# Optimization experiments

Measured on AMD Instinct MI355X. Metric: run time of the kernel, lower is better.

Reference implementation:

```python
import jax, jax.numpy as jnp
import numpy as np

NUM_LEVELS = 16
COARSEST = 16
FINEST = 1024
TABLE_SIZE = 524288  # max_hash_table_entries per level
FEAT = 2             # hash_table_feature_dim
DENSITY_W = 64
COLOR_W = 64
N_POINTS = 262144

PRIMES = jnp.array([1, 2654435761, 805459861], dtype=jnp.uint32)
# 8 cube corners: 1 -> ceil coordinate, 0 -> floor coordinate (matches source vertex_0..vertex_7)
CORNER_SEL = np.array([[1,1,1],[1,1,0],[1,0,1],[0,1,1],[1,0,0],[0,1,0],[0,0,1],[0,0,0]], dtype=bool)


def hash_encode(position, hash_table):
    # position: (N,3) in [0,1); hash_table: (NUM_LEVELS*TABLE_SIZE, FEAT)
    levels = jnp.arange(NUM_LEVELS)
    growth = jnp.exp((jnp.log(float(FINEST)) - jnp.log(float(COARSEST))) / (NUM_LEVELS - 1))
    scalings = jnp.floor(COARSEST * growth ** levels)            # (L,)
    scaled = position[:, None, :] * scalings[None, :, None]       # (N,L,3)
    floor = jnp.floor(scaled)
    ceil = jnp.ceil(scaled)
    sel = jnp.asarray(CORNER_SEL)[None, None]                     # (1,1,8,3)
    corners = jnp.where(sel, ceil[:, :, None, :], floor[:, :, None, :]).astype(jnp.uint32)  # (N,L,8,3)
    h = corners * PRIMES                                          # uint32 wrap-around mul
    idx = jnp.bitwise_xor(jnp.bitwise_xor(h[..., 0], h[..., 1]), h[..., 2]) % TABLE_SIZE
    idx = idx + (levels[None, :, None] * TABLE_SIZE).astype(jnp.uint32)  # (N,L,8)
    feats = hash_table[idx]                                       # (N,L,8,F) gather
    frac = scaled - floor                                         # (N,L,3)
    w = jnp.prod(jnp.where(sel, frac[:, :, None, :], 1.0 - frac[:, :, None, :]), axis=-1)  # (N,L,8)
    out = jnp.sum(feats * w[..., None], axis=2)                   # trilinear interp -> (N,L,F)
    return out.reshape(out.shape[0], NUM_LEVELS * FEAT)           # (N,32)


def sh_encode(d):
    # fourth-order spherical harmonics, vectorized over (N,3)
    x, y, z = d[:, 0], d[:, 1], d[:, 2]
    xx, yy, zz = x * x, y * y, z * z
    comps = [
        0.28209479177387814 * jnp.ones_like(x),
        0.4886025119029199 * y,
        0.4886025119029199 * z,
        0.4886025119029199 * x,
        1.0925484305920792 * x * y,
        1.0925484305920792 * y * z,
        0.9461746957575601 * zz - 0.31539156525252,
        1.0925484305920792 * x * z,
        0.5462742152960396 * (xx - yy),
        0.5900435899266435 * y * (3 * xx - yy),
        2.890611442640554 * x * y * z,
        0.4570457994644658 * y * (5 * zz - 1),
        0.3731763325901154 * z * (5 * zz - 3),
        0.4570457994644658 * x * (5 * zz - 1),
        1.445305721320277 * z * (xx - yy),
        0.5900435899266435 * x * (xx - 3 * yy),
    ]
    return jnp.stack(comps, axis=-1)  # (N,16)


def setup_inputs() -> dict:
    key = jax.random.key(0)
    ks = jax.random.split(key, 16)
    N = N_POINTS
    position = jax.random.uniform(ks[0], (N, 3), dtype=jnp.float32)
    direction = jax.random.normal(ks[1], (N, 3), dtype=jnp.float32)
    hash_table = jax.random.normal(ks[2], (NUM_LEVELS * TABLE_SIZE, FEAT), dtype=jnp.float32) * 1e-2
    enc_dim = NUM_LEVELS * FEAT  # 32
    def dense(k, fi, fo):
        return jax.random.normal(k, (fi, fo), dtype=jnp.float32) * (1.0 / np.sqrt(fi))
    return {
        "position": position,
        "direction": direction,
        "hash_table": hash_table,
        "w_d1": dense(ks[3], enc_dim, DENSITY_W), "b_d1": jnp.zeros((DENSITY_W,), jnp.float32),
        "w_d2": dense(ks[4], DENSITY_W, 16),      "b_d2": jnp.zeros((16,), jnp.float32),
        "w_c1": dense(ks[5], 16 + 16, COLOR_W),   "b_c1": jnp.zeros((COLOR_W,), jnp.float32),
        "w_c2": dense(ks[6], COLOR_W, COLOR_W),   "b_c2": jnp.zeros((COLOR_W,), jnp.float32),
        "w_c3": dense(ks[7], COLOR_W, 3),         "b_c3": jnp.zeros((3,), jnp.float32),
    }


def reference(position, direction, hash_table, w_d1, b_d1, w_d2, b_d2,
              w_c1, b_c1, w_c2, b_c2, w_c3, b_c3):
    enc_pos = hash_encode(position, hash_table)               # (N,32)
    h = jax.nn.relu(enc_pos @ w_d1 + b_d1)                    # (N,64)
    density = h @ w_d2 + b_d2                                 # (N,16)
    enc_dir = sh_encode(direction)                            # (N,16)
    x = jnp.concatenate([density, enc_dir], axis=-1)          # (N,32)
    x = jax.nn.relu(x @ w_c1 + b_c1)
    x = jax.nn.relu(x @ w_c2 + b_c2)
    x = x @ w_c3 + b_c3                                       # (N,3)
    color = jax.nn.sigmoid(x)                                 # high_dynamic_range=False
    return (density, color)
```

## Files before the change

### kernel.cpp

```cpp
#include <hip/hip_runtime.h>
#include <stdint.h>

#define NPTS 262144
#define TBL 524288u
#define TBL_MASK 524287u

#define WS_TAB_BYTES (16u * 524288u * 4u)
#define WS_ENC_OFF   WS_TAB_BYTES
#define WS_ENC_BYTES (16u * (uint32_t)NPTS * 4u)
#define WS_NEED      ((size_t)WS_TAB_BYTES + (size_t)WS_ENC_BYTES)

typedef __attribute__((ext_vector_type(8))) _Float16 half8;
typedef __attribute__((ext_vector_type(4))) float f32x4;

__device__ const float d_scale[16] = {16.f, 21.f, 27.f, 36.f, 48.f, 64.f, 84.f, 111.f,
                                      147.f, 194.f, 256.f, 337.f, 445.f, 588.f, 776.f, 1024.f};

__device__ __forceinline__ uint16_t f2h(float f) {
    _Float16 h = (_Float16)f;
    return __builtin_bit_cast(uint16_t, h);
}
__device__ __forceinline__ uint32_t pack2(float lo, float hi) {
    return (uint32_t)f2h(lo) | ((uint32_t)f2h(hi) << 16);
}
__device__ __forceinline__ float h2f_lo(uint32_t v) {
    return (float)__builtin_bit_cast(_Float16, (uint16_t)(v & 0xffffu));
}
__device__ __forceinline__ float h2f_hi(uint32_t v) {
    return (float)__builtin_bit_cast(_Float16, (uint16_t)(v >> 16));
}

__device__ __forceinline__ half8 bfrag(const float* __restrict__ W, int N, int kofs, int nofs, int l) {
    const int k0 = kofs + ((l >> 4) << 3);
    const float* p = W + (size_t)k0 * N + (nofs + (l & 15));
    union { uint32_t u[4]; half8 s; } r;
    r.u[0] = pack2(p[0 * N], p[1 * N]);
    r.u[1] = pack2(p[2 * N], p[3 * N]);
    r.u[2] = pack2(p[4 * N], p[5 * N]);
    r.u[3] = pack2(p[6 * N], p[7 * N]);
    return r.s;
}

__device__ __forceinline__ half8 bfrag3(const float* __restrict__ W, int kofs, int l) {
    const int k0 = kofs + ((l >> 4) << 3);
    const int n = l & 15;
    union { uint32_t u[4]; half8 s; } r;
    if (n < 3) {
        const float* p = W + (size_t)k0 * 3 + n;
        r.u[0] = pack2(p[0],  p[3]);
        r.u[1] = pack2(p[6],  p[9]);
        r.u[2] = pack2(p[12], p[15]);
        r.u[3] = pack2(p[18], p[21]);
    } else {
        r.u[0] = 0; r.u[1] = 0; r.u[2] = 0; r.u[3] = 0;
    }
    return r.s;
}

__device__ __forceinline__ half8 ld_a_h(const unsigned char* hcb, int mt, int kb, int l) {
    const int row = mt * 16 + (l & 15);
    uint32_t byte = (uint32_t)row * 128 + (uint32_t)kb * 64 + (uint32_t)((l >> 4) << 4);
    byte ^= (uint32_t)(row & 7) << 4;
    return *(const half8*)(hcb + byte);
}

__device__ __forceinline__ void st_h(unsigned char* hcb, int row, int col, float v) {
    uint32_t byte = (uint32_t)row * 128 + (uint32_t)col * 2;
    byte ^= (uint32_t)(row & 7) << 4;
    *(uint16_t*)(hcb + byte) = f2h(fmaxf(v, 0.f));
}

#define MFMA(a, b, c) __builtin_amdgcn_mfma_f32_16x16x32_f16((a), (b), (c), 0, 0, 0)

__global__ void __launch_bounds__(256) convert_tab(
    const float4* __restrict__ t, uint4* __restrict__ o, int n4)
{
    const int i = blockIdx.x * 256 + threadIdx.x;
    if (i < n4) {
        const float4 a = t[2 * i];
        const float4 b = t[2 * i + 1];
        o[i] = make_uint4(pack2(a.x, a.y), pack2(a.z, a.w),
                          pack2(b.x, b.y), pack2(b.z, b.w));
    }
}

__global__ void __launch_bounds__(256) gather_enc(
    const float* __restrict__ g_pos,
    const uint32_t* __restrict__ tab16,
    uint32_t* __restrict__ enc)
{
    const int b = blockIdx.x;
    const int x8 = b & 7;
    const int lev = (b >> 13) ? (15 - x8) : x8;
    const int p = (((b >> 3) & 1023) << 8) + threadIdx.x;

    const float px = g_pos[3 * p + 0];
    const float py = g_pos[3 * p + 1];
    const float pz = g_pos[3 * p + 2];

    const float s = d_scale[lev];
    const float sx = px * s, sy = py * s, sz = pz * s;
    const float fx = floorf(sx), fy = floorf(sy), fz = floorf(sz);
    const float cx = ceilf(sx),  cy = ceilf(sy),  cz = ceilf(sz);
    const float tx = sx - fx, ty = sy - fy, tz = sz - fz;
    const uint32_t x0 = (uint32_t)fx, x1 = (uint32_t)cx;
    const uint32_t hy0 = (uint32_t)fy * 2654435761u, hy1 = (uint32_t)cy * 2654435761u;
    const uint32_t hz0 = (uint32_t)fz * 805459861u,  hz1 = (uint32_t)cz * 805459861u;
    const bool xodd = (x0 & 1u) != 0u;

    const uint32_t* t = tab16 + (size_t)lev * TBL;
    float e0 = 0.f, e1 = 0.f;
    #pragma unroll
    for (int cp = 0; cp < 4; ++cp) {
        const uint32_t hyz = ((cp & 1) ? hy1 : hy0) ^ ((cp & 2) ? hz1 : hz0);
        const uint32_t idx0 = (x0 ^ hyz) & TBL_MASK;
        const uint32_t idx1 = (x1 ^ hyz) & TBL_MASK;
        const uint2 v2 = *reinterpret_cast<const uint2*>(t + (idx0 & ~1u));
        const bool lo = (idx0 & 1u) == 0u;
        const uint32_t v0 = lo ? v2.x : v2.y;
        uint32_t v1 = lo ? v2.y : v2.x;
        if (xodd) v1 = t[idx1];
        const float wyz = ((cp & 1) ? ty : 1.f - ty) * ((cp & 2) ? tz : 1.f - tz);
        const float w0 = (1.f - tx) * wyz;
        const float w1 = tx * wyz;
        e0 = fmaf(h2f_lo(v0), w0, fmaf(h2f_lo(v1), w1, e0));
        e1 = fmaf(h2f_hi(v0), w0, fmaf(h2f_hi(v1), w1, e1));
    }
    enc[(size_t)lev * NPTS + p] = pack2(e0, e1);
}

__global__ void __launch_bounds__(256, 3) nerf_mlp(
    const float* __restrict__ g_dir,
    const uint32_t* __restrict__ enc,
    const float* __restrict__ g_wd1,
    const float* __restrict__ g_bd1,
    const float* __restrict__ g_wd2,
    const float* __restrict__ g_bd2,
    const float* __restrict__ g_wc1,
    const float* __restrict__ g_bc1,
    const float* __restrict__ g_wc2,
    const float* __restrict__ g_bc2,
    const float* __restrict__ g_wc3,
    const float* __restrict__ g_bc3,
    float* __restrict__ g_out)
{
    __shared__ __align__(16) unsigned char s_lds[4 * 12288];
    unsigned char* wbase = s_lds + (threadIdx.x >> 6) * 12288;
    unsigned char* hcb  = wbase;
    unsigned char* xinb = wbase + 8192;

    const int l = threadIdx.x & 63;
    const int m_my = l >> 4;
    const int r_my = l & 15;
    const int wpt  = blockIdx.x * 256 + (threadIdx.x & 192);
    const int p    = wpt + l;

    #pragma unroll
    for (int kb = 0; kb < 4; ++kb) {
        uint4 w4;
        w4.x = enc[(size_t)(4 * kb + 0) * NPTS + p];
        w4.y = enc[(size_t)(4 * kb + 1) * NPTS + p];
        w4.z = enc[(size_t)(4 * kb + 2) * NPTS + p];
        w4.w = enc[(size_t)(4 * kb + 3) * NPTS + p];
        *(uint4*)(hcb + m_my * 1024 + (kb * 16 + r_my) * 16) = w4;
    }

    const float dx = g_dir[3 * p + 0];
    const float dy = g_dir[3 * p + 1];
    const float dz = g_dir[3 * p + 2];

    {
        const float xx = dx * dx, yy = dy * dy, zz = dz * dz;
        float s[16];
        s[0]  = 0.28209479177387814f;
        s[1]  = 0.4886025119029199f * dy;
        s[2]  = 0.4886025119029199f * dz;
        s[3]  = 0.4886025119029199f * dx;
        s[4]  = 1.0925484305920792f * dx * dy;
        s[5]  = 1.0925484305920792f * dy * dz;
        s[6]  = 0.9461746957575601f * zz - 0.31539156525252f;
        s[7]  = 1.0925484305920792f * dx * dz;
        s[8]  = 0.5462742152960396f * (xx - yy);
        s[9]  = 0.5900435899266435f * dy * (3.f * xx - yy);
        s[10] = 2.890611442640554f * dx * dy * dz;
        s[11] = 0.4570457994644658f * dy * (5.f * zz - 1.f);
        s[12] = 0.3731763325901154f * dz * (5.f * zz - 3.f);
        s[13] = 0.4570457994644658f * dx * (5.f * zz - 1.f);
        s[14] = 1.445305721320277f * dz * (xx - yy);
        s[15] = 0.5900435899266435f * dx * (xx - 3.f * yy);
        *(uint4*)(xinb + m_my * 1024 + (32 + r_my) * 16) =
            make_uint4(pack2(s[0], s[1]), pack2(s[2], s[3]), pack2(s[4], s[5]), pack2(s[6], s[7]));
        *(uint4*)(xinb + m_my * 1024 + (48 + r_my) * 16) =
            make_uint4(pack2(s[8], s[9]), pack2(s[10], s[11]), pack2(s[12], s[13]), pack2(s[14], s[15]));
    }

    const int cl = l & 15;
    const int rg = (l >> 4) << 2;

    {
        f32x4 acc[4][4];
        half8 B[4];
        #pragma unroll
        for (int nt = 0; nt < 4; ++nt) {
            B[nt] = bfrag(g_wd1, 64, 0, nt * 16, l);
            const float b = g_bd1[nt * 16 + cl];
            #pragma unroll
            for (int mt = 0; mt < 4; ++mt) acc[mt][nt] = (f32x4){b, b, b, b};
        }
        #pragma unroll
        for (int mt = 0; mt < 4; ++mt) {
            const half8 A = *(const half8*)(hcb + mt * 1024 + l * 16);
            #pragma unroll
            for (int nt = 0; nt < 4; ++nt) acc[mt][nt] = MFMA(A, B[nt], acc[mt][nt]);
        }
        #pragma unroll
        for (int mt = 0; mt < 4; ++mt)
            #pragma unroll
            for (int nt = 0; nt < 4; ++nt)
                #pragma unroll
                for (int r = 0; r < 4; ++r)
                    st_h(hcb, mt * 16 + rg + r, nt * 16 + cl, acc[mt][nt][r]);
    }

    {
        const half8 B0 = bfrag(g_wd2, 16, 0,  0, l);
        const half8 B1 = bfrag(g_wd2, 16, 32, 0, l);
        const float b = g_bd2[cl];
        #pragma unroll
        for (int mt = 0; mt < 4; ++mt) {
            f32x4 acc = (f32x4){b, b, b, b};
            acc = MFMA(ld_a_h(hcb, mt, 0, l), B0, acc);
            acc = MFMA(ld_a_h(hcb, mt, 1, l), B1, acc);
            #pragma unroll
            for (int r = 0; r < 4; ++r) {
                const int pt = wpt + mt * 16 + rg + r;
                g_out[(size_t)pt * 16 + cl] = acc[r];
                const uint32_t byte = (uint32_t)mt * 1024
                                    + (uint32_t)(((cl >> 3) * 16 + rg + r) * 16) + (uint32_t)(cl & 7) * 2;
                *(uint16_t*)(xinb + byte) = f2h(acc[r]);
            }
        }
    }

    {
        f32x4 acc[4][4];
        half8 B[4];
        #pragma unroll
        for (int nt = 0; nt < 4; ++nt) {
            B[nt] = bfrag(g_wc1, 64, 0, nt * 16, l);
            const float b = g_bc1[nt * 16 + cl];
            #pragma unroll
            for (int mt = 0; mt < 4; ++mt) acc[mt][nt] = (f32x4){b, b, b, b};
        }
        #pragma unroll
        for (int mt = 0; mt < 4; ++mt) {
            const half8 A = *(const half8*)(xinb + mt * 1024 + l * 16);
            #pragma unroll
            for (int nt = 0; nt < 4; ++nt) acc[mt][nt] = MFMA(A, B[nt], acc[mt][nt]);
        }
        #pragma unroll
        for (int mt = 0; mt < 4; ++mt)
            #pragma unroll
            for (int nt = 0; nt < 4; ++nt)
                #pragma unroll
                for (int r = 0; r < 4; ++r)
                    st_h(hcb, mt * 16 + rg + r, nt * 16 + cl, acc[mt][nt][r]);
    }

    {
        f32x4 acc[4][4];
        #pragma unroll
        for (int nt = 0; nt < 4; ++nt) {
            const float b = g_bc2[nt * 16 + cl];
            #pragma unroll
            for (int mt = 0; mt < 4; ++mt) acc[mt][nt] = (f32x4){b, b, b, b};
        }
        #pragma unroll
        for (int kb = 0; kb < 2; ++kb) {
            half8 A[4];
            #pragma unroll
            for (int mt = 0; mt < 4; ++mt) A[mt] = ld_a_h(hcb, mt, kb, l);
            #pragma unroll
            for (int nt = 0; nt < 4; ++nt) {
                const half8 B = bfrag(g_wc2, 64, kb * 32, nt * 16, l);
                #pragma unroll
                for (int mt = 0; mt < 4; ++mt) acc[mt][nt] = MFMA(A[mt], B, acc[mt][nt]);
            }
        }
        #pragma unroll
        for (int mt = 0; mt < 4; ++mt)
            #pragma unroll
            for (int nt = 0; nt < 4; ++nt)
                #pragma unroll
                for (int r = 0; r < 4; ++r)
                    st_h(hcb, mt * 16 + rg + r, nt * 16 + cl, acc[mt][nt][r]);
    }

    {
        const half8 B0 = bfrag3(g_wc3, 0, l);
        const half8 B1 = bfrag3(g_wc3, 32, l);
        const float b = (cl < 3) ? g_bc3[cl] : 0.f;
        #pragma unroll
        for (int mt = 0; mt < 4; ++mt) {
            f32x4 acc = (f32x4){b, b, b, b};
            acc = MFMA(ld_a_h(hcb, mt, 0, l), B0, acc);
            acc = MFMA(ld_a_h(hcb, mt, 1, l), B1, acc);
            if (cl < 3) {
                #pragma unroll
                for (int r = 0; r < 4; ++r) {
                    const int pt = wpt + mt * 16 + rg + r;
                    g_out[(size_t)NPTS * 16 + (size_t)pt * 3 + cl] = 1.f / (1.f + expf(-acc[r]));
                }
            }
        }
    }
}

__global__ void __launch_bounds__(256, 3) nerf_fused(
    const float* __restrict__ g_pos,
    const float* __restrict__ g_dir,
    const float* __restrict__ g_tab,
    const float* __restrict__ g_wd1,
    const float* __restrict__ g_bd1,
    const float* __restrict__ g_wd2,
    const float* __restrict__ g_bd2,
    const float* __restrict__ g_wc1,
    const float* __restrict__ g_bc1,
    const float* __restrict__ g_wc2,
    const float* __restrict__ g_bc2,
    const float* __restrict__ g_wc3,
    const float* __restrict__ g_bc3,
    float* __restrict__ g_out)
{
    __shared__ __align__(16) unsigned char s_lds[4 * 12288];
    unsigned char* wbase = s_lds + (threadIdx.x >> 6) * 12288;
    unsigned char* hcb  = wbase;
    unsigned char* xinb = wbase + 8192;

    const int l = threadIdx.x & 63;
    const int m_my = l >> 4;
    const int r_my = l & 15;
    const int wpt  = blockIdx.x * 256 + (threadIdx.x & 192);
    const int p    = wpt + l;

    const float px = g_pos[3 * p + 0];
    const float py = g_pos[3 * p + 1];
    const float pz = g_pos[3 * p + 2];
    const float dx = g_dir[3 * p + 0];
    const float dy = g_dir[3 * p + 1];
    const float dz = g_dir[3 * p + 2];

    constexpr float scale[16] = {16.f, 21.f, 27.f, 36.f, 48.f, 64.f, 84.f, 111.f,
                                 147.f, 194.f, 256.f, 337.f, 445.f, 588.f, 776.f, 1024.f};

    #pragma unroll
    for (int kb = 0; kb < 4; ++kb) {
        uint32_t w[4];
        #pragma unroll
        for (int l4 = 0; l4 < 4; ++l4) {
            const int lev = kb * 4 + l4;
            const float s = scale[lev];
            const float sx = px * s, sy = py * s, sz = pz * s;
            const float fx = floorf(sx), fy = floorf(sy), fz = floorf(sz);
            const float cx = ceilf(sx),  cy = ceilf(sy),  cz = ceilf(sz);
            const float tx = sx - fx, ty = sy - fy, tz = sz - fz;
            const uint32_t x0 = (uint32_t)fx, x1 = (uint32_t)cx;
            const uint32_t hy0 = (uint32_t)fy * 2654435761u, hy1 = (uint32_t)cy * 2654435761u;
            const uint32_t hz0 = (uint32_t)fz * 805459861u,  hz1 = (uint32_t)cz * 805459861u;
            const uint32_t base = (uint32_t)lev * TBL;
            float e0 = 0.f, e1 = 0.f;
            #pragma unroll
            for (int c = 0; c < 8; ++c) {
                const uint32_t hx = (c & 1) ? x1 : x0;
                const uint32_t hy = (c & 2) ? hy1 : hy0;
                const uint32_t hz = (c & 4) ? hz1 : hz0;
                const uint32_t idx = ((hx ^ hy ^ hz) & TBL_MASK) + base;
                const float2 fv = *reinterpret_cast<const float2*>(g_tab + 2 * (size_t)idx);
                const float wgt = ((c & 1) ? tx : 1.f - tx)
                                * ((c & 2) ? ty : 1.f - ty)
                                * ((c & 4) ? tz : 1.f - tz);
                e0 = fmaf(fv.x, wgt, e0);
                e1 = fmaf(fv.y, wgt, e1);
            }
            w[l4] = pack2(e0, e1);
        }
        *(uint4*)(hcb + m_my * 1024 + (kb * 16 + r_my) * 16) = make_uint4(w[0], w[1], w[2], w[3]);
    }

    {
        const float xx = dx * dx, yy = dy * dy, zz = dz * dz;
        float s[16];
        s[0]  = 0.28209479177387814f;
        s[1]  = 0.4886025119029199f * dy;
        s[2]  = 0.4886025119029199f * dz;
        s[3]  = 0.4886025119029199f * dx;
        s[4]  = 1.0925484305920792f * dx * dy;
        s[5]  = 1.0925484305920792f * dy * dz;
        s[6]  = 0.9461746957575601f * zz - 0.31539156525252f;
        s[7]  = 1.0925484305920792f * dx * dz;
        s[8]  = 0.5462742152960396f * (xx - yy);
        s[9]  = 0.5900435899266435f * dy * (3.f * xx - yy);
        s[10] = 2.890611442640554f * dx * dy * dz;
        s[11] = 0.4570457994644658f * dy * (5.f * zz - 1.f);
        s[12] = 0.3731763325901154f * dz * (5.f * zz - 3.f);
        s[13] = 0.4570457994644658f * dx * (5.f * zz - 1.f);
        s[14] = 1.445305721320277f * dz * (xx - yy);
        s[15] = 0.5900435899266435f * dx * (xx - 3.f * yy);
        *(uint4*)(xinb + m_my * 1024 + (32 + r_my) * 16) =
            make_uint4(pack2(s[0], s[1]), pack2(s[2], s[3]), pack2(s[4], s[5]), pack2(s[6], s[7]));
        *(uint4*)(xinb + m_my * 1024 + (48 + r_my) * 16) =
            make_uint4(pack2(s[8], s[9]), pack2(s[10], s[11]), pack2(s[12], s[13]), pack2(s[14], s[15]));
    }

    const int cl = l & 15;
    const int rg = (l >> 4) << 2;

    {
        f32x4 acc[4][4];
        half8 B[4];
        #pragma unroll
        for (int nt = 0; nt < 4; ++nt) {
            B[nt] = bfrag(g_wd1, 64, 0, nt * 16, l);
            const float b = g_bd1[nt * 16 + cl];
            #pragma unroll
            for (int mt = 0; mt < 4; ++mt) acc[mt][nt] = (f32x4){b, b, b, b};
        }
        #pragma unroll
        for (int mt = 0; mt < 4; ++mt) {
            const half8 A = *(const half8*)(hcb + mt * 1024 + l * 16);
            #pragma unroll
            for (int nt = 0; nt < 4; ++nt) acc[mt][nt] = MFMA(A, B[nt], acc[mt][nt]);
        }
        #pragma unroll
        for (int mt = 0; mt < 4; ++mt)
            #pragma unroll
            for (int nt = 0; nt < 4; ++nt)
                #pragma unroll
                for (int r = 0; r < 4; ++r)
                    st_h(hcb, mt * 16 + rg + r, nt * 16 + cl, acc[mt][nt][r]);
    }

    {
        const half8 B0 = bfrag(g_wd2, 16, 0,  0, l);
        const half8 B1 = bfrag(g_wd2, 16, 32, 0, l);
        const float b = g_bd2[cl];
        #pragma unroll
        for (int mt = 0; mt < 4; ++mt) {
            f32x4 acc = (f32x4){b, b, b, b};
            acc = MFMA(ld_a_h(hcb, mt, 0, l), B0, acc);
            acc = MFMA(ld_a_h(hcb, mt, 1, l), B1, acc);
            #pragma unroll
            for (int r = 0; r < 4; ++r) {
                const int pt = wpt + mt * 16 + rg + r;
                g_out[(size_t)pt * 16 + cl] = acc[r];
                const uint32_t byte = (uint32_t)mt * 1024
                                    + (uint32_t)(((cl >> 3) * 16 + rg + r) * 16) + (uint32_t)(cl & 7) * 2;
                *(uint16_t*)(xinb + byte) = f2h(acc[r]);
            }
        }
    }

    {
        f32x4 acc[4][4];
        half8 B[4];
        #pragma unroll
        for (int nt = 0; nt < 4; ++nt) {
            B[nt] = bfrag(g_wc1, 64, 0, nt * 16, l);
            const float b = g_bc1[nt * 16 + cl];
            #pragma unroll
            for (int mt = 0; mt < 4; ++mt) acc[mt][nt] = (f32x4){b, b, b, b};
        }
        #pragma unroll
        for (int mt = 0; mt < 4; ++mt) {
            const half8 A = *(const half8*)(xinb + mt * 1024 + l * 16);
            #pragma unroll
            for (int nt = 0; nt < 4; ++nt) acc[mt][nt] = MFMA(A, B[nt], acc[mt][nt]);
        }
        #pragma unroll
        for (int mt = 0; mt < 4; ++mt)
            #pragma unroll
            for (int nt = 0; nt < 4; ++nt)
                #pragma unroll
                for (int r = 0; r < 4; ++r)
                    st_h(hcb, mt * 16 + rg + r, nt * 16 + cl, acc[mt][nt][r]);
    }

    {
        f32x4 acc[4][4];
        #pragma unroll
        for (int nt = 0; nt < 4; ++nt) {
            const float b = g_bc2[nt * 16 + cl];
            #pragma unroll
            for (int mt = 0; mt < 4; ++mt) acc[mt][nt] = (f32x4){b, b, b, b};
        }
        #pragma unroll
        for (int kb = 0; kb < 2; ++kb) {
            half8 A[4];
            #pragma unroll
            for (int mt = 0; mt < 4; ++mt) A[mt] = ld_a_h(hcb, mt, kb, l);
            #pragma unroll
            for (int nt = 0; nt < 4; ++nt) {
                const half8 B = bfrag(g_wc2, 64, kb * 32, nt * 16, l);
                #pragma unroll
                for (int mt = 0; mt < 4; ++mt) acc[mt][nt] = MFMA(A[mt], B, acc[mt][nt]);
            }
        }
        #pragma unroll
        for (int mt = 0; mt < 4; ++mt)
            #pragma unroll
            for (int nt = 0; nt < 4; ++nt)
                #pragma unroll
                for (int r = 0; r < 4; ++r)
                    st_h(hcb, mt * 16 + rg + r, nt * 16 + cl, acc[mt][nt][r]);
    }

    {
        const half8 B0 = bfrag3(g_wc3, 0, l);
        const half8 B1 = bfrag3(g_wc3, 32, l);
        const float b = (cl < 3) ? g_bc3[cl] : 0.f;
        #pragma unroll
        for (int mt = 0; mt < 4; ++mt) {
            f32x4 acc = (f32x4){b, b, b, b};
            acc = MFMA(ld_a_h(hcb, mt, 0, l), B0, acc);
            acc = MFMA(ld_a_h(hcb, mt, 1, l), B1, acc);
            if (cl < 3) {
                #pragma unroll
                for (int r = 0; r < 4; ++r) {
                    const int pt = wpt + mt * 16 + rg + r;
                    g_out[(size_t)NPTS * 16 + (size_t)pt * 3 + cl] = 1.f / (1.f + expf(-acc[r]));
                }
            }
        }
    }
}

extern "C" void kernel_launch(void* const* d_in, const int* in_sizes, int n_in,
                              void* d_out, int out_size, void* d_ws, size_t ws_size,
                              hipStream_t stream) {
    if (ws_size >= WS_NEED) {
        uint32_t* tab16 = (uint32_t*)d_ws;
        uint32_t* enc   = (uint32_t*)((char*)d_ws + WS_ENC_OFF);
        convert_tab<<<8192, 256, 0, stream>>>(
            (const float4*)d_in[2], (uint4*)tab16, 2097152);
        gather_enc<<<16384, 256, 0, stream>>>(
            (const float*)d_in[0], tab16, enc);
        nerf_mlp<<<NPTS / 256, 256, 0, stream>>>(
            (const float*)d_in[1], enc,
            (const float*)d_in[3], (const float*)d_in[4],
            (const float*)d_in[5], (const float*)d_in[6],
            (const float*)d_in[7], (const float*)d_in[8],
            (const float*)d_in[9], (const float*)d_in[10],
            (const float*)d_in[11], (const float*)d_in[12],
            (float*)d_out);
    } else {
        nerf_fused<<<NPTS / 256, 256, 0, stream>>>(
            (const float*)d_in[0], (const float*)d_in[1], (const float*)d_in[2],
            (const float*)d_in[3], (const float*)d_in[4],
            (const float*)d_in[5], (const float*)d_in[6],
            (const float*)d_in[7], (const float*)d_in[8],
            (const float*)d_in[9], (const float*)d_in[10],
            (const float*)d_in[11], (const float*)d_in[12],
            (float*)d_out);
    }
}
```

Before: 159.5 us.

## Pre-pack MLP weights to fp16 once and batch two points per gather thread

Block 0 of the table-conversion kernel now packs all MLP weight matrices into fp16 pairs in workspace. The MLP kernel then loads B fragments as ready-made uint32 pairs instead of doing eight strided fp32 loads and conversions per fragment in every block. The gather kernel is rewritten so each thread handles two points, issuing all hash-table loads before using them to raise memory-level parallelism. The workspace requirement grows a little, and extra serial work lands on one block of the conversion kernel.

New measurement: 157.1 us. About the same (-1.5%).

```diff
diff --git a/kernel.cpp b/kernel.cpp
--- a/kernel.cpp
+++ b/kernel.cpp
@@ -8,7 +8,15 @@
 #define WS_TAB_BYTES (16u * 524288u * 4u)
 #define WS_ENC_OFF   WS_TAB_BYTES
 #define WS_ENC_BYTES (16u * (uint32_t)NPTS * 4u)
-#define WS_NEED      ((size_t)WS_TAB_BYTES + (size_t)WS_ENC_BYTES)
+#define WS_W_OFF     ((size_t)WS_TAB_BYTES + (size_t)WS_ENC_BYTES)
+#define WS_W_U32     4736
+#define WS_NEED      (WS_W_OFF + (size_t)WS_W_U32 * 4u)
+
+#define PW_D1 0
+#define PW_D2 1024
+#define PW_C1 1536
+#define PW_C2 2560
+#define PW_C3 4608
 
 typedef __attribute__((ext_vector_type(8))) _Float16 half8;
 typedef __attribute__((ext_vector_type(4))) float f32x4;
@@ -28,6 +36,33 @@
 }
 __device__ __forceinline__ float h2f_hi(uint32_t v) {
     return (float)__builtin_bit_cast(_Float16, (uint16_t)(v >> 16));
+}
+
+__device__ __forceinline__ half8 bfrag_p(const uint32_t* __restrict__ Wp, int N, int kofs, int nofs, int l) {
+    const int kp0 = (kofs + ((l >> 4) << 3)) >> 1;
+    const uint32_t* p = Wp + (size_t)kp0 * N + (nofs + (l & 15));
+    union { uint32_t u[4]; half8 s; } r;
+    r.u[0] = p[0 * N];
+    r.u[1] = p[1 * N];
+    r.u[2] = p[2 * N];
+    r.u[3] = p[3 * N];
+    return r.s;
+}
+
+__device__ __forceinline__ half8 bfrag3_p(const uint32_t* __restrict__ Wp, int kofs, int l) {
+    const int kp0 = (kofs + ((l >> 4) << 3)) >> 1;
+    const int n = l & 15;
+    union { uint32_t u[4]; half8 s; } r;
+    if (n < 3) {
+        const uint32_t* p = Wp + (size_t)kp0 * 4 + n;
+        r.u[0] = p[0];
+        r.u[1] = p[4];
+        r.u[2] = p[8];
+        r.u[3] = p[12];
+    } else {
+        r.u[0] = 0; r.u[1] = 0; r.u[2] = 0; r.u[3] = 0;
+    }
+    return r.s;
 }
 
 __device__ __forceinline__ half8 bfrag(const float* __restrict__ W, int N, int kofs, int nofs, int l) {
@@ -40,7 +75,6 @@
     r.u[3] = pack2(p[6 * N], p[7 * N]);
     return r.s;
 }
-
 __device__ __forceinline__ half8 bfrag3(const float* __restrict__ W, int kofs, int l) {
     const int k0 = kofs + ((l >> 4) << 3);
     const int n = l & 15;
@@ -73,7 +107,10 @@
 #define MFMA(a, b, c) __builtin_amdgcn_mfma_f32_16x16x32_f16((a), (b), (c), 0, 0, 0)
 
 __global__ void __launch_bounds__(256) convert_tab(
-    const float4* __restrict__ t, uint4* __restrict__ o, int n4)
+    const float4* __restrict__ t, uint4* __restrict__ o, int n4,
+    const float* __restrict__ wd1, const float* __restrict__ wd2,
+    const float* __restrict__ wc1, const float* __restrict__ wc2,
+    const float* __restrict__ wc3, uint32_t* __restrict__ wp)
 {
     const int i = blockIdx.x * 256 + threadIdx.x;
     if (i < n4) {
@@ -82,65 +119,106 @@
         o[i] = make_uint4(pack2(a.x, a.y), pack2(a.z, a.w),
                           pack2(b.x, b.y), pack2(b.z, b.w));
     }
-}
-
-__global__ void __launch_bounds__(256) gather_enc(
+    if (blockIdx.x == 0) {
+        const int tid = threadIdx.x;
+        for (int j = tid; j < 1024; j += 256) {
+            const int kp = j >> 6, n = j & 63;
+            wp[PW_D1 + j] = pack2(wd1[(2 * kp) * 64 + n], wd1[(2 * kp + 1) * 64 + n]);
+        }
+        for (int j = tid; j < 512; j += 256) {
+            const int kp = j >> 4, n = j & 15;
+            wp[PW_D2 + j] = pack2(wd2[(2 * kp) * 16 + n], wd2[(2 * kp + 1) * 16 + n]);
+        }
+        for (int j = tid; j < 1024; j += 256) {
+            const int kp = j >> 6, n = j & 63;
+            wp[PW_C1 + j] = pack2(wc1[(2 * kp) * 64 + n], wc1[(2 * kp + 1) * 64 + n]);
+        }
+        for (int j = tid; j < 2048; j += 256) {
+            const int kp = j >> 6, n = j & 63;
+            wp[PW_C2 + j] = pack2(wc2[(2 * kp) * 64 + n], wc2[(2 * kp + 1) * 64 + n]);
+        }
+        for (int j = tid; j < 128; j += 256) {
+            const int kp = j >> 2, n = j & 3;
+            wp[PW_C3 + j] = (n < 3) ? pack2(wc3[(2 * kp) * 3 + n], wc3[(2 * kp + 1) * 3 + n]) : 0u;
+        }
+    }
+}
+
+__global__ void __launch_bounds__(256) gather_enc2(
     const float* __restrict__ g_pos,
     const uint32_t* __restrict__ tab16,
     uint32_t* __restrict__ enc)
 {
     const int b = blockIdx.x;
     const int x8 = b & 7;
-    const int lev = (b >> 13) ? (15 - x8) : x8;
-    const int p = (((b >> 3) & 1023) << 8) + threadIdx.x;
-
-    const float px = g_pos[3 * p + 0];
-    const float py = g_pos[3 * p + 1];
-    const float pz = g_pos[3 * p + 2];
+    const int lev = (b >> 12) ? (15 - x8) : x8;
+    const int pbase = (((b >> 3) & 511) << 9) + threadIdx.x;
 
     const float s = d_scale[lev];
-    const float sx = px * s, sy = py * s, sz = pz * s;
-    const float fx = floorf(sx), fy = floorf(sy), fz = floorf(sz);
-    const float cx = ceilf(sx),  cy = ceilf(sy),  cz = ceilf(sz);
-    const float tx = sx - fx, ty = sy - fy, tz = sz - fz;
-    const uint32_t x0 = (uint32_t)fx, x1 = (uint32_t)cx;
-    const uint32_t hy0 = (uint32_t)fy * 2654435761u, hy1 = (uint32_t)cy * 2654435761u;
-    const uint32_t hz0 = (uint32_t)fz * 805459861u,  hz1 = (uint32_t)cz * 805459861u;
-    const bool xodd = (x0 & 1u) != 0u;
-
     const uint32_t* t = tab16 + (size_t)lev * TBL;
-    float e0 = 0.f, e1 = 0.f;
+
+    float tx[2], ty[2], tz[2];
+    uint32_t idx0[2][4], idx1[2][4];
+    bool odd[2];
     #pragma unroll
-    for (int cp = 0; cp < 4; ++cp) {
-        const uint32_t hyz = ((cp & 1) ? hy1 : hy0) ^ ((cp & 2) ? hz1 : hz0);
-        const uint32_t idx0 = (x0 ^ hyz) & TBL_MASK;
-        const uint32_t idx1 = (x1 ^ hyz) & TBL_MASK;
-        const uint2 v2 = *reinterpret_cast<const uint2*>(t + (idx0 & ~1u));
-        const bool lo = (idx0 & 1u) == 0u;
-        const uint32_t v0 = lo ? v2.x : v2.y;
-        uint32_t v1 = lo ? v2.y : v2.x;
-        if (xodd) v1 = t[idx1];
-        const float wyz = ((cp & 1) ? ty : 1.f - ty) * ((cp & 2) ? tz : 1.f - tz);
-        const float w0 = (1.f - tx) * wyz;
-        const float w1 = tx * wyz;
-        e0 = fmaf(h2f_lo(v0), w0, fmaf(h2f_lo(v1), w1, e0));
-        e1 = fmaf(h2f_hi(v0), w0, fmaf(h2f_hi(v1), w1, e1));
-    }
-    enc[(size_t)lev * NPTS + p] = pack2(e0, e1);
+    for (int q = 0; q < 2; ++q) {
+        const int p = pbase + q * 256;
+        const float px = g_pos[3 * p + 0];
+        const float py = g_pos[3 * p + 1];
+        const float pz = g_pos[3 * p + 2];
+        const float sx = px * s, sy = py * s, sz = pz * s;
+        const float fx = floorf(sx), fy = floorf(sy), fz = floorf(sz);
+        tx[q] = sx - fx; ty[q] = sy - fy; tz[q] = sz - fz;
+        const uint32_t x0 = (uint32_t)fx, x1 = (uint32_t)ceilf(sx);
+        const uint32_t hy0 = (uint32_t)fy * 2654435761u, hy1 = (uint32_t)ceilf(sy) * 2654435761u;
+        const uint32_t hz0 = (uint32_t)fz * 805459861u,  hz1 = (uint32_t)ceilf(sz) * 805459861u;
+        odd[q] = (x0 & 1u) != 0u;
+        #pragma unroll
+        for (int cp = 0; cp < 4; ++cp) {
+            const uint32_t hyz = ((cp & 1) ? hy1 : hy0) ^ ((cp & 2) ? hz1 : hz0);
+            idx0[q][cp] = (x0 ^ hyz) & TBL_MASK;
+            idx1[q][cp] = (x1 ^ hyz) & TBL_MASK;
+        }
+    }
+    uint2 v2[2][4];
+    #pragma unroll
+    for (int q = 0; q < 2; ++q)
+        #pragma unroll
+        for (int cp = 0; cp < 4; ++cp)
+            v2[q][cp] = *reinterpret_cast<const uint2*>(t + (idx0[q][cp] & ~1u));
+    uint32_t fup[2][4];
+    #pragma unroll
+    for (int q = 0; q < 2; ++q)
+        #pragma unroll
+        for (int cp = 0; cp < 4; ++cp)
+            fup[q][cp] = odd[q] ? t[idx1[q][cp]] : 0u;
+    #pragma unroll
+    for (int q = 0; q < 2; ++q) {
+        float e0 = 0.f, e1 = 0.f;
+        #pragma unroll
+        for (int cp = 0; cp < 4; ++cp) {
+            const bool lo = (idx0[q][cp] & 1u) == 0u;
+            const uint32_t v0 = lo ? v2[q][cp].x : v2[q][cp].y;
+            uint32_t v1 = lo ? v2[q][cp].y : v2[q][cp].x;
+            if (odd[q]) v1 = fup[q][cp];
+            const float wyz = ((cp & 1) ? ty[q] : 1.f - ty[q]) * ((cp & 2) ? tz[q] : 1.f - tz[q]);
+            const float w0 = (1.f - tx[q]) * wyz;
+            const float w1 = tx[q] * wyz;
+            e0 = fmaf(h2f_lo(v0), w0, fmaf(h2f_lo(v1), w1, e0));
+            e1 = fmaf(h2f_hi(v0), w0, fmaf(h2f_hi(v1), w1, e1));
+        }
+        enc[(size_t)lev * NPTS + pbase + q * 256] = pack2(e0, e1);
+    }
 }
 
 __global__ void __launch_bounds__(256, 3) nerf_mlp(
     const float* __restrict__ g_dir,
     const uint32_t* __restrict__ enc,
-    const float* __restrict__ g_wd1,
+    const uint32_t* __restrict__ wp,
     const float* __restrict__ g_bd1,
-    const float* __restrict__ g_wd2,
     const float* __restrict__ g_bd2,
-    const float* __restrict__ g_wc1,
     const float* __restrict__ g_bc1,
-    const float* __restrict__ g_wc2,
     const float* __restrict__ g_bc2,
-    const float* __restrict__ g_wc3,
     const float* __restrict__ g_bc3,
     float* __restrict__ g_out)
 {
@@ -202,7 +280,7 @@
         half8 B[4];
         #pragma unroll
         for (int nt = 0; nt < 4; ++nt) {
-            B[nt] = bfrag(g_wd1, 64, 0, nt * 16, l);
+            B[nt] = bfrag_p(wp + PW_D1, 64, 0, nt * 16, l);
             const float b = g_bd1[nt * 16 + cl];
             #pragma unroll
             for (int mt = 0; mt < 4; ++mt) acc[mt][nt] = (f32x4){b, b, b, b};
@@ -223,8 +301,8 @@
     }
 
     {
-        const half8 B0 = bfrag(g_wd2, 16, 0,  0, l);
-        const half8 B1 = bfrag(g_wd2, 16, 32, 0, l);
+        const half8 B0 = bfrag_p(wp + PW_D2, 16, 0,  0, l);
+        const half8 B1 = bfrag_p(wp + PW_D2, 16, 32, 0, l);
         const float b = g_bd2[cl];
         #pragma unroll
         for (int mt = 0; mt < 4; ++mt) {
@@ -247,7 +325,7 @@
         half8 B[4];
         #pragma unroll
         for (int nt = 0; nt < 4; ++nt) {
-            B[nt] = bfrag(g_wc1, 64, 0, nt * 16, l);
+            B[nt] = bfrag_p(wp + PW_C1, 64, 0, nt * 16, l);
             const float b = g_bc1[nt * 16 + cl];
             #pragma unroll
             for (int mt = 0; mt < 4; ++mt) acc[mt][nt] = (f32x4){b, b, b, b};
@@ -282,7 +360,7 @@
             for (int mt = 0; mt < 4; ++mt) A[mt] = ld_a_h(hcb, mt, kb, l);
             #pragma unroll
             for (int nt = 0; nt < 4; ++nt) {
-                const half8 B = bfrag(g_wc2, 64, kb * 32, nt * 16, l);
+                const half8 B = bfrag_p(wp + PW_C2, 64, kb * 32, nt * 16, l);
                 #pragma unroll
                 for (int mt = 0; mt < 4; ++mt) acc[mt][nt] = MFMA(A[mt], B, acc[mt][nt]);
             }
@@ -297,8 +375,8 @@
     }
 
     {
-        const half8 B0 = bfrag3(g_wc3, 0, l);
-        const half8 B1 = bfrag3(g_wc3, 32, l);
+        const half8 B0 = bfrag3_p(wp + PW_C3, 0, l);
+        const half8 B1 = bfrag3_p(wp + PW_C3, 32, l);
         const float b = (cl < 3) ? g_bc3[cl] : 0.f;
         #pragma unroll
         for (int mt = 0; mt < 4; ++mt) {
@@ -540,17 +618,19 @@
     if (ws_size >= WS_NEED) {
         uint32_t* tab16 = (uint32_t*)d_ws;
         uint32_t* enc   = (uint32_t*)((char*)d_ws + WS_ENC_OFF);
+        uint32_t* wpk   = (uint32_t*)((char*)d_ws + WS_W_OFF);
         convert_tab<<<8192, 256, 0, stream>>>(
-            (const float4*)d_in[2], (uint4*)tab16, 2097152);
-        gather_enc<<<16384, 256, 0, stream>>>(
+            (const float4*)d_in[2], (uint4*)tab16, 2097152,
+            (const float*)d_in[3], (const float*)d_in[5],
+            (const float*)d_in[7], (const float*)d_in[9],
+            (const float*)d_in[11], wpk);
+        gather_enc2<<<8192, 256, 0, stream>>>(
             (const float*)d_in[0], tab16, enc);
         nerf_mlp<<<NPTS / 256, 256, 0, stream>>>(
-            (const float*)d_in[1], enc,
-            (const float*)d_in[3], (const float*)d_in[4],
-            (const float*)d_in[5], (const float*)d_in[6],
-            (const float*)d_in[7], (const float*)d_in[8],
-            (const float*)d_in[9], (const float*)d_in[10],
-            (const float*)d_in[11], (const float*)d_in[12],
+            (const float*)d_in[1], enc, wpk,
+            (const float*)d_in[4], (const float*)d_in[6],
+            (const float*)d_in[8], (const float*)d_in[10],
+            (const float*)d_in[12],
             (float*)d_out);
     } else {
         nerf_fused<<<NPTS / 256, 256, 0, stream>>>(
```
